# Optimization experiments

Measured on AMD Instinct MI355X. Metric: run time of the kernel, lower is better.

The kernel has to match this reference:

```python
import jax, jax.numpy as jnp
import numpy as np

S_SIGMA = 8      # spatial downsampling of the bilateral grid
N_BINS = 16      # intensity bins (range resolution)
EPS = 1e-8


def _blur_axis(g, k, axis):
    """1D correlation of grid g with small tap filter k along `axis` (zero pad)."""
    taps = k.shape[0]
    r = taps // 2
    pad = [(0, 0)] * g.ndim
    pad[axis] = (r, r)
    gp = jnp.pad(g, pad)
    n = g.shape[axis]
    out = k[0] * jax.lax.slice_in_dim(gp, 0, n, axis=axis)
    for i in range(1, taps):
        out = out + k[i] * jax.lax.slice_in_dim(gp, i, i + n, axis=axis)
    return out


def _bilateral_one(img, fs, fr):
    """Bilateral grid splat -> blur -> slice for a single [H,W] channel.
    Guide signal is the channel itself (values assumed in [0,1])."""
    H, W = img.shape
    GH = (H - 1) // S_SIGMA + 2
    GW = (W - 1) // S_SIGMA + 2
    GZ = N_BINS + 1

    ys = jnp.arange(H, dtype=img.dtype)
    xs = jnp.arange(W, dtype=img.dtype)

    # ---- splat (nearest-cell scatter-add of homogeneous (value, weight)) ----
    gy = jnp.round(ys / S_SIGMA).astype(jnp.int32)            # [H]
    gx = jnp.round(xs / S_SIGMA).astype(jnp.int32)            # [W]
    gyg, gxg = jnp.meshgrid(gy, gx, indexing='ij')            # [H,W]
    gz = jnp.clip(jnp.round(img * (N_BINS - 1)), 0, N_BINS - 1).astype(jnp.int32)
    val = jnp.zeros((GH, GW, GZ), img.dtype).at[gyg, gxg, gz].add(img)
    wt = jnp.zeros((GH, GW, GZ), img.dtype).at[gyg, gxg, gz].add(jnp.ones_like(img))

    # ---- blur grid: learnable 5-tap filter_s along y,x and filter_r along z ----
    for axis, k in ((0, fs), (1, fs), (2, fr)):
        val = _blur_axis(val, k, axis)
        wt = _blur_axis(wt, k, axis)

    # ---- slice (trilinear gather at (y/s, x/s, I*(NB-1))) ----
    fy = ys / S_SIGMA
    fx = xs / S_SIGMA
    fz = jnp.clip(img * (N_BINS - 1), 0.0, N_BINS - 1)        # [H,W]
    y0 = jnp.floor(fy).astype(jnp.int32)
    x0 = jnp.floor(fx).astype(jnp.int32)
    z0 = jnp.floor(fz).astype(jnp.int32)
    y1 = jnp.minimum(y0 + 1, GH - 1)
    x1 = jnp.minimum(x0 + 1, GW - 1)
    z1 = jnp.minimum(z0 + 1, GZ - 1)
    ty = fy - y0.astype(img.dtype)                            # [H]
    tx = fx - x0.astype(img.dtype)                            # [W]
    tz = fz - z0.astype(img.dtype)                            # [H,W]

    out_v = jnp.zeros_like(img)
    out_w = jnp.zeros_like(img)
    for yi, wy in ((y0, 1.0 - ty), (y1, ty)):
        for xi, wx in ((x0, 1.0 - tx), (x1, tx)):
            for zi, wz in ((z0, 1.0 - tz), (z1, tz)):
                w = wy[:, None] * wx[None, :] * wz            # [H,W]
                out_v = out_v + w * val[yi[:, None], xi[None, :], zi]
                out_w = out_w + w * wt[yi[:, None], xi[None, :], zi]
    return out_v / (out_w + EPS)


def setup_inputs() -> dict:
    key = jax.random.key(0)
    k1, k2 = jax.random.split(key)
    blurred_batch = jax.random.uniform(k1, (4, 3, 1024, 1024), dtype=jnp.float32)
    kernel_batch = jax.random.uniform(k2, (4, 11, 11), dtype=jnp.float32)
    g = jnp.array([1.0, 4.0, 6.0, 4.0, 1.0], dtype=jnp.float32)
    g = g / g.sum()  # smooth 5-tap filter so the blur is nontrivial
    return {
        'blurred_batch': blurred_batch,
        'kernel_batch': kernel_batch,
        'filter_s': g,
        'filter_r': g,
        'num_irls_iter': 1,
        'num_cg_iter': 5,
    }


def reference(blurred_batch, kernel_batch, filter_s, filter_r, num_irls_iter, num_cg_iter):
    # kernel_batch, num_irls_iter, num_cg_iter are unused on this code path,
    # matching the original forward (only BilateralGrid.apply touches x).
    B, C, H, W = blurred_batch.shape
    imgs = blurred_batch.reshape(B * C, H, W)
    out = jax.vmap(lambda im: _bilateral_one(im, filter_s, filter_r))(imgs)
    return out.reshape(B, C, H, W)
```

## Files before the change

### kernel.cpp

```cpp
#include <hip/hip_runtime.h>

#define S_SIGMA 8
#define NBINS   16
#define HDIM    1024
#define WDIM    1024
#define GH      129
#define GW      129
#define GZ      17
#define CELLS   (GH*GW*GZ)
#define ROWSZ   (GW*GZ)
#define EPSV    1e-8f
#define FIXS    1048576.0f
#define FIXI    (1.0f/1048576.0f)


__global__ __launch_bounds__(256) void splat_gather_kernel(
    const float* __restrict__ img, float* __restrict__ grid, int nImg, int imgBase)
{
    __shared__ unsigned lval[16 * 32];
    __shared__ unsigned lwt [16 * 32];

    int tid = threadIdx.x;
    int c   = tid & 31;
    int h   = tid >> 5;
    int cellIdx = blockIdx.x * 32 + c;
    int total = nImg * GH * GW;

    for (int i = tid; i < 16 * 32; i += 256) { lval[i] = 0u; lwt[i] = 0u; }
    __syncthreads();

    if (cellIdx < total) {
        int b   = cellIdx / (GH * GW);
        int rem = cellIdx - b * (GH * GW);
        int gy  = rem / GW;
        int gx  = rem - gy * GW;
        const float* ib = img + (size_t)(imgBase + b) * (HDIM * WDIM);

        bool interior = (gx >= 1) & (gx <= 127) & (gy >= 1) & (gy <= 127);
        if (interior) {
            int py = gy & 1, px = gx & 1;
            int ylo = 8 * gy - 4 + py;
            int nr  = 9 - 2 * py;
            int ax  = 8 * gx - 4;
            for (int r = h; r < nr; r += 8) {
                const float* rp = ib + (size_t)(ylo + r) * WDIM + ax;
                float4 A = *(const float4*)rp;
                float4 B = *(const float4*)(rp + 4);
                float  cv = rp[8];
                float e7[7] = {A.y, A.z, A.w, B.x, B.y, B.z, B.w};
                #pragma unroll
                for (int j = 0; j < 7; ++j) {
                    float v = e7[j];
                    int gz = min(max((int)rintf(v * 15.0f), 0), 15);
                    atomicAdd(&lval[gz * 32 + c], (unsigned)rintf(v * FIXS));
                    atomicAdd(&lwt [gz * 32 + c], 1u);
                }
                if (!px) {
                    int gz = min(max((int)rintf(A.x * 15.0f), 0), 15);
                    atomicAdd(&lval[gz * 32 + c], (unsigned)rintf(A.x * FIXS));
                    atomicAdd(&lwt [gz * 32 + c], 1u);
                    gz = min(max((int)rintf(cv * 15.0f), 0), 15);
                    atomicAdd(&lval[gz * 32 + c], (unsigned)rintf(cv * FIXS));
                    atomicAdd(&lwt [gz * 32 + c], 1u);
                }
            }
        } else {
            int ylo = max(0, 8 * gy - 4 + (gy & 1));
            int yhi = min(HDIM - 1, 8 * gy + 4 - (gy & 1));
            int xlo = max(0, 8 * gx - 4 + (gx & 1));
            int xhi = min(WDIM - 1, 8 * gx + 4 - (gx & 1));
            for (int y = ylo + h; y <= yhi; y += 8) {
                const float* row = ib + (size_t)y * WDIM;
                for (int x = xlo; x <= xhi; ++x) {
                    float v = row[x];
                    int gz = min(max((int)rintf(v * 15.0f), 0), 15);
                    atomicAdd(&lval[gz * 32 + c], (unsigned)rintf(v * FIXS));
                    atomicAdd(&lwt [gz * 32 + c], 1u);
                }
            }
        }
    }
    __syncthreads();

    if (cellIdx < total) {
        float2* dst = (float2*)grid + (size_t)cellIdx * GZ;
        int zlo = 2 * h;
        int zhi = (h == 7) ? 17 : zlo + 2;
        for (int z = zlo; z < zhi; ++z) {
            float2 o;
            if (z == 16) { o.x = 0.f; o.y = 0.f; }
            else {
                o.x = (float)lval[z * 32 + c] * FIXI;
                o.y = (float)lwt [z * 32 + c];
            }
            dst[z] = o;
        }
    }
}

__global__ __launch_bounds__(256) void blur_y_row(
    const float2* __restrict__ in, float2* __restrict__ out,
    const float* __restrict__ kfs)
{
    int i  = blockIdx.x * 256 + threadIdx.x;
    if (i >= ROWSZ) return;
    int gy = blockIdx.y;
    int b  = blockIdx.z;

    float ks[5] = {kfs[0], kfs[1], kfs[2], kfs[3], kfs[4]};

    const float2* gb = in + (size_t)b * CELLS + i;
    float2 a; a.x = 0.f; a.y = 0.f;
    #pragma unroll
    for (int t = 0; t < 5; ++t) {
        int yy = gy + t - 2;
        if (yy >= 0 && yy < GH) {
            float2 g = gb[(size_t)yy * ROWSZ];
            a.x += ks[t] * g.x;
            a.y += ks[t] * g.y;
        }
    }
    out[(size_t)b * CELLS + (size_t)gy * ROWSZ + i] = a;
}

#define NRI 9

__global__ __launch_bounds__(256) void blur_xz_row(
    const float2* __restrict__ in, float2* __restrict__ out,
    const float* __restrict__ kfs, const float* __restrict__ kfr)
{
    __shared__ float2 sbin[ROWSZ];

    int tid = threadIdx.x;
    int gy  = blockIdx.x;
    int b   = blockIdx.y;

    float ks[5] = {kfs[0], kfs[1], kfs[2], kfs[3], kfs[4]};
    float kr[5] = {kfr[0], kfr[1], kfr[2], kfr[3], kfr[4]};

    const float2* gsrc = in + (size_t)b * CELLS + (size_t)gy * ROWSZ;
    for (int i = tid; i < ROWSZ; i += 256) sbin[i] = gsrc[i];
    __syncthreads();

    float2 rt[NRI];
    #pragma unroll
    for (int it = 0; it < NRI; ++it) {
        int o = tid + it * 256;
        float2 a; a.x = 0.f; a.y = 0.f;
        if (o < ROWSZ) {
            int gx = o / GZ;
            #pragma unroll
            for (int t = 0; t < 5; ++t) {
                int xx = gx + t - 2;
                if (xx >= 0 && xx < GW) {
                    float2 g = sbin[o + (t - 2) * GZ];
                    a.x += ks[t] * g.x;
                    a.y += ks[t] * g.y;
                }
            }
        }
        rt[it] = a;
    }
    __syncthreads();
    #pragma unroll
    for (int it = 0; it < NRI; ++it) {
        int o = tid + it * 256;
        if (o < ROWSZ) sbin[o] = rt[it];
    }
    __syncthreads();

    float2* ob = out + (size_t)b * CELLS + (size_t)gy * ROWSZ;
    for (int o2 = tid; o2 < ROWSZ; o2 += 256) {
        int z  = o2 / GW;
        int gx = o2 - z * GW;
        float2 a; a.x = 0.f; a.y = 0.f;
        #pragma unroll
        for (int t = 0; t < 5; ++t) {
            int zz = z + t - 2;
            if (zz >= 0 && zz < GZ) {
                float2 g = sbin[gx * GZ + zz];
                a.x += kr[t] * g.x;
                a.y += kr[t] * g.y;
            }
        }
        ob[o2] = a;
    }
}

#define XP2   136
#define RST   XP2
#define ZST   (2*XP2)

__global__ __launch_bounds__(256) void slice_rows_kernel(
    const float* __restrict__ img, const float2* __restrict__ grid,
    float* __restrict__ out, int imgBase)
{
    __shared__ float2 sg[GZ * ZST];

    int tid = threadIdx.x;
    int k   = blockIdx.x;
    int b   = blockIdx.y;

    const float2* gsrc = grid + (size_t)b * CELLS + (size_t)k * ROWSZ;
    for (int i = tid; i < 2 * ROWSZ; i += 256) {
        int r   = i / ROWSZ;
        int rem = i - r * ROWSZ;
        int z   = rem / GW;
        int x0  = rem - z * GW;
        sg[z * ZST + r * RST + x0] = gsrc[i];
    }
    __syncthreads();

    int x   = tid << 2;
    int x0v = tid >> 1;
    float txb = (float)(x & 7) * 0.125f;

    size_t rowBase = (size_t)(imgBase + b) * (HDIM * WDIM) + (size_t)(k << 3) * WDIM + x;

    #pragma unroll
    for (int r = 0; r < 8; ++r) {
        size_t pixBase = rowBase + (size_t)r * WDIM;
        float4 v4 = *(const float4*)(img + pixBase);
        float ty = (float)r * 0.125f;
        float wy0 = 1.f - ty, wy1 = ty;

        float vv[4] = {v4.x, v4.y, v4.z, v4.w};
        float rr[4];
        #pragma unroll
        for (int j = 0; j < 4; ++j) {
            float v  = vv[j];
            float fz = fminf(fmaxf(v * 15.0f, 0.0f), 15.0f);
            float zf = floorf(fz);
            int   z0 = (int)zf;
            float tz = fz - zf;
            float tx = txb + (float)j * 0.125f;
            float wx0 = 1.f - tx, wx1 = tx;
            float wz0 = 1.f - tz, wz1 = tz;

            int base = z0 * ZST + x0v;
            float2 g000 = sg[base];
            float2 g010 = sg[base + 1];
            float2 g100 = sg[base + RST];
            float2 g110 = sg[base + RST + 1];
            float2 g001 = sg[base + ZST];
            float2 g011 = sg[base + ZST + 1];
            float2 g101 = sg[base + ZST + RST];
            float2 g111 = sg[base + ZST + RST + 1];

            float ov = 0.f, ow = 0.f, w;
            w = wy0 * wx0 * wz0; ov += w * g000.x; ow += w * g000.y;
            w = wy0 * wx0 * wz1; ov += w * g001.x; ow += w * g001.y;
            w = wy0 * wx1 * wz0; ov += w * g010.x; ow += w * g010.y;
            w = wy0 * wx1 * wz1; ov += w * g011.x; ow += w * g011.y;
            w = wy1 * wx0 * wz0; ov += w * g100.x; ow += w * g100.y;
            w = wy1 * wx0 * wz1; ov += w * g101.x; ow += w * g101.y;
            w = wy1 * wx1 * wz0; ov += w * g110.x; ow += w * g110.y;
            w = wy1 * wx1 * wz1; ov += w * g111.x; ow += w * g111.y;
            rr[j] = ov / (ow + EPSV);
        }
        float4 r4; r4.x = rr[0]; r4.y = rr[1]; r4.z = rr[2]; r4.w = rr[3];
        *(float4*)(out + pixBase) = r4;
    }
}

extern "C" void kernel_launch(void* const* d_in, const int* in_sizes, int n_in,
                              void* d_out, int out_size, void* d_ws, size_t ws_size,
                              hipStream_t stream)
{
    const float* img = (const float*)d_in[0];
    const float* fs  = (const float*)d_in[2];
    const float* fr  = (const float*)d_in[3];
    float* out = (float*)d_out;

    int nImgTotal = in_sizes[0] / (HDIM * WDIM);
    size_t perImgBytes = (size_t)CELLS * 2 * sizeof(float);

    int maxChunk = (int)(ws_size / (2 * perImgBytes));
    if (maxChunk < 1) return;
    if (maxChunk > nImgTotal) maxChunk = nImgTotal;

    for (int base = 0; base < nImgTotal; base += maxChunk) {
        int c = nImgTotal - base;
        if (c > maxChunk) c = maxChunk;

        float* A = (float*)d_ws;
        float* B = A + (size_t)c * CELLS * 2;

        int nCells = c * GH * GW;
        int cellBlocks = (nCells + 31) / 32;
        splat_gather_kernel<<<cellBlocks, 256, 0, stream>>>(img, A, c, base);

        dim3 ygrid((ROWSZ + 255) / 256, GH, c);
        blur_y_row<<<ygrid, 256, 0, stream>>>((const float2*)A, (float2*)B, fs);

        dim3 xzgrid(GH, c);
        blur_xz_row<<<xzgrid, 256, 0, stream>>>((const float2*)B, (float2*)A, fs, fr);

        dim3 sgrid(HDIM / 8, c);
        slice_rows_kernel<<<sgrid, 256, 0, stream>>>(img, (const float2*)A, out, base);
    }
}
```

Before: 96.15 us.

## Fuse y-blur into xz-blur kernel and widen splat blocks to 64 cells

The separate y-axis blur kernel is removed; the xz blur kernel now computes the 5-tap y blur while loading each grid row into shared memory, which removes one launch and a full grid write and read. The slice kernel reads the result from the second buffer. Separately, the splat kernel now handles 64 cells per block with 4 row-groups instead of 32 cells with 8, giving each thread more rows to process and doubling LDS histogram size.

```diff
diff --git a/kernel.cpp b/kernel.cpp
--- a/kernel.cpp
+++ b/kernel.cpp
@@ -17,16 +17,16 @@
 __global__ __launch_bounds__(256) void splat_gather_kernel(
     const float* __restrict__ img, float* __restrict__ grid, int nImg, int imgBase)
 {
-    __shared__ unsigned lval[16 * 32];
-    __shared__ unsigned lwt [16 * 32];
+    __shared__ unsigned lval[16 * 64];
+    __shared__ unsigned lwt [16 * 64];
 
     int tid = threadIdx.x;
-    int c   = tid & 31;
-    int h   = tid >> 5;
-    int cellIdx = blockIdx.x * 32 + c;
+    int c   = tid & 63;
+    int q   = tid >> 6;
+    int cellIdx = blockIdx.x * 64 + c;
     int total = nImg * GH * GW;
 
-    for (int i = tid; i < 16 * 32; i += 256) { lval[i] = 0u; lwt[i] = 0u; }
+    for (int i = tid; i < 16 * 64; i += 256) { lval[i] = 0u; lwt[i] = 0u; }
     __syncthreads();
 
     if (cellIdx < total) {
@@ -42,7 +42,7 @@
             int ylo = 8 * gy - 4 + py;
             int nr  = 9 - 2 * py;
             int ax  = 8 * gx - 4;
-            for (int r = h; r < nr; r += 8) {
+            for (int r = q; r < nr; r += 4) {
                 const float* rp = ib + (size_t)(ylo + r) * WDIM + ax;
                 float4 A = *(const float4*)rp;
                 float4 B = *(const float4*)(rp + 4);
@@ -52,16 +52,16 @@
                 for (int j = 0; j < 7; ++j) {
                     float v = e7[j];
                     int gz = min(max((int)rintf(v * 15.0f), 0), 15);
-                    atomicAdd(&lval[gz * 32 + c], (unsigned)rintf(v * FIXS));
-                    atomicAdd(&lwt [gz * 32 + c], 1u);
+                    atomicAdd(&lval[gz * 64 + c], (unsigned)rintf(v * FIXS));
+                    atomicAdd(&lwt [gz * 64 + c], 1u);
                 }
                 if (!px) {
                     int gz = min(max((int)rintf(A.x * 15.0f), 0), 15);
-                    atomicAdd(&lval[gz * 32 + c], (unsigned)rintf(A.x * FIXS));
-                    atomicAdd(&lwt [gz * 32 + c], 1u);
+                    atomicAdd(&lval[gz * 64 + c], (unsigned)rintf(A.x * FIXS));
+                    atomicAdd(&lwt [gz * 64 + c], 1u);
                     gz = min(max((int)rintf(cv * 15.0f), 0), 15);
-                    atomicAdd(&lval[gz * 32 + c], (unsigned)rintf(cv * FIXS));
-                    atomicAdd(&lwt [gz * 32 + c], 1u);
+                    atomicAdd(&lval[gz * 64 + c], (unsigned)rintf(cv * FIXS));
+                    atomicAdd(&lwt [gz * 64 + c], 1u);
                 }
             }
         } else {
@@ -69,13 +69,13 @@
             int yhi = min(HDIM - 1, 8 * gy + 4 - (gy & 1));
             int xlo = max(0, 8 * gx - 4 + (gx & 1));
             int xhi = min(WDIM - 1, 8 * gx + 4 - (gx & 1));
-            for (int y = ylo + h; y <= yhi; y += 8) {
+            for (int y = ylo + q; y <= yhi; y += 4) {
                 const float* row = ib + (size_t)y * WDIM;
                 for (int x = xlo; x <= xhi; ++x) {
                     float v = row[x];
                     int gz = min(max((int)rintf(v * 15.0f), 0), 15);
-                    atomicAdd(&lval[gz * 32 + c], (unsigned)rintf(v * FIXS));
-                    atomicAdd(&lwt [gz * 32 + c], 1u);
+                    atomicAdd(&lval[gz * 64 + c], (unsigned)rintf(v * FIXS));
+                    atomicAdd(&lwt [gz * 64 + c], 1u);
                 }
             }
         }
@@ -84,48 +84,23 @@
 
     if (cellIdx < total) {
         float2* dst = (float2*)grid + (size_t)cellIdx * GZ;
-        int zlo = 2 * h;
-        int zhi = (h == 7) ? 17 : zlo + 2;
+        int zlo = q * 4;
+        int zhi = (q == 3) ? 17 : zlo + 4;
         for (int z = zlo; z < zhi; ++z) {
             float2 o;
             if (z == 16) { o.x = 0.f; o.y = 0.f; }
             else {
-                o.x = (float)lval[z * 32 + c] * FIXI;
-                o.y = (float)lwt [z * 32 + c];
+                o.x = (float)lval[z * 64 + c] * FIXI;
+                o.y = (float)lwt [z * 64 + c];
             }
             dst[z] = o;
         }
     }
 }
 
-__global__ __launch_bounds__(256) void blur_y_row(
-    const float2* __restrict__ in, float2* __restrict__ out,
-    const float* __restrict__ kfs)
-{
-    int i  = blockIdx.x * 256 + threadIdx.x;
-    if (i >= ROWSZ) return;
-    int gy = blockIdx.y;
-    int b  = blockIdx.z;
-
-    float ks[5] = {kfs[0], kfs[1], kfs[2], kfs[3], kfs[4]};
-
-    const float2* gb = in + (size_t)b * CELLS + i;
-    float2 a; a.x = 0.f; a.y = 0.f;
-    #pragma unroll
-    for (int t = 0; t < 5; ++t) {
-        int yy = gy + t - 2;
-        if (yy >= 0 && yy < GH) {
-            float2 g = gb[(size_t)yy * ROWSZ];
-            a.x += ks[t] * g.x;
-            a.y += ks[t] * g.y;
-        }
-    }
-    out[(size_t)b * CELLS + (size_t)gy * ROWSZ + i] = a;
-}
-
 #define NRI 9
 
-__global__ __launch_bounds__(256) void blur_xz_row(
+__global__ __launch_bounds__(256) void blur_yxz_row(
     const float2* __restrict__ in, float2* __restrict__ out,
     const float* __restrict__ kfs, const float* __restrict__ kfr)
 {
@@ -138,8 +113,18 @@
     float ks[5] = {kfs[0], kfs[1], kfs[2], kfs[3], kfs[4]};
     float kr[5] = {kfr[0], kfr[1], kfr[2], kfr[3], kfr[4]};
 
-    const float2* gsrc = in + (size_t)b * CELLS + (size_t)gy * ROWSZ;
-    for (int i = tid; i < ROWSZ; i += 256) sbin[i] = gsrc[i];
+    const float2* gb = in + (size_t)b * CELLS;
+    int ylo = max(0, gy - 2), yhi = min(GH - 1, gy + 2);
+    for (int i = tid; i < ROWSZ; i += 256) {
+        float2 a; a.x = 0.f; a.y = 0.f;
+        for (int yy = ylo; yy <= yhi; ++yy) {
+            float k = ks[yy - gy + 2];
+            float2 g = gb[(size_t)yy * ROWSZ + i];
+            a.x += k * g.x;
+            a.y += k * g.y;
+        }
+        sbin[i] = a;
+    }
     __syncthreads();
 
     float2 rt[NRI];
@@ -287,16 +272,13 @@
         float* B = A + (size_t)c * CELLS * 2;
 
         int nCells = c * GH * GW;
-        int cellBlocks = (nCells + 31) / 32;
+        int cellBlocks = (nCells + 63) / 64;
         splat_gather_kernel<<<cellBlocks, 256, 0, stream>>>(img, A, c, base);
 
-        dim3 ygrid((ROWSZ + 255) / 256, GH, c);
-        blur_y_row<<<ygrid, 256, 0, stream>>>((const float2*)A, (float2*)B, fs);
-
-        dim3 xzgrid(GH, c);
-        blur_xz_row<<<xzgrid, 256, 0, stream>>>((const float2*)B, (float2*)A, fs, fr);
+        dim3 bgrid(GH, c);
+        blur_yxz_row<<<bgrid, 256, 0, stream>>>((const float2*)A, (float2*)B, fs, fr);
 
         dim3 sgrid(HDIM / 8, c);
-        slice_rows_kernel<<<sgrid, 256, 0, stream>>>(img, (const float2*)A, out, base);
-    }
-}
+        slice_rows_kernel<<<sgrid, 256, 0, stream>>>(img, (const float2*)B, out, base);
+    }
+}
```

Measured after the change: 92.31 us. 4.0% less time.
